# Kernel optimization log

Measured on AMD Instinct MI355X. Metric: run time of the kernel, lower is better.

The kernel has to match this reference:

```python
import jax, jax.numpy as jnp
import numpy as np

N_QUBITS = 8
DEPTH = 2
DIM = 2 ** N_QUBITS

# Hadamard gate (symmetric)
_H = (1.0 / np.sqrt(2.0)) * jnp.array([[1.0, 1.0], [1.0, -1.0]], dtype=jnp.complex64)
# sign table for <Z_i>: bit of wire i is bit (n-1-i) of the basis index (wire 0 = MSB)
_bits = (np.arange(DIM)[:, None] >> np.arange(N_QUBITS - 1, -1, -1)[None, :]) & 1
_SIGNS = jnp.asarray(1.0 - 2.0 * _bits, dtype=jnp.float32)  # [DIM, n_qubits]


def _quantum(ang):
    """Vectorized statevector simulation of the circuit:
    RX(ang_i) on each wire, then DEPTH x (CNOT ladder + H on last wire);
    returns <Z_i> for each wire. ang: [R, N_QUBITS] float32 -> [R, N_QUBITS]."""
    R = ang.shape[0]
    half = ang * 0.5
    a0 = jnp.cos(half).astype(jnp.complex64)
    a1 = (jnp.sin(half) * (-1j)).astype(jnp.complex64)  # RX|0> = cos|0> - i sin|1>
    single = jnp.stack([a0, a1], axis=-1)  # [R, n, 2]
    # product state via kron over qubits (wire 0 is the most significant factor)
    state = single[:, 0]  # [R, 2]
    for q in range(1, N_QUBITS):
        state = (state[:, :, None] * single[:, q][:, None, :]).reshape(R, -1)
    for _ in range(DEPTH):
        # CNOT ladder on adjacent wires (i -> i+1)
        for i in range(N_QUBITS - 1):
            s = state.reshape(R, 2 ** i, 2, 2, -1)  # [R, pre, ctrl, tgt, post]
            s = jnp.concatenate([s[:, :, :1], s[:, :, 1:, ::-1]], axis=2)
            state = s.reshape(R, -1)
        # Hadamard on the last wire
        s = state.reshape(R, -1, 2)
        state = (s @ _H).reshape(R, -1)
    probs = state.real ** 2 + state.imag ** 2  # [R, DIM]
    return probs @ _SIGNS  # [R, n_qubits]


def setup_inputs() -> dict:
    key = jax.random.key(0)
    k_x, k_w1, k_w2 = jax.random.split(key, 3)
    B, S, E, F = 8, 4096, 1024, N_QUBITS
    x = jax.random.normal(k_x, (B, S, E), dtype=jnp.float32)
    w1 = jax.random.normal(k_w1, (F, E), dtype=jnp.float32) * 0.02
    b1 = jnp.zeros((F,), dtype=jnp.float32)
    w2 = jax.random.normal(k_w2, (E, F), dtype=jnp.float32) * 0.02
    b2 = jnp.zeros((E,), dtype=jnp.float32)
    return {"x": x, "w1": w1, "b1": b1, "w2": w2, "b2": b2}


def reference(x, w1, b1, w2, b2):
    B, S, E = x.shape
    h = jnp.einsum('bse,fe->bsf', x, w1) + b1  # linear1 -> [B, S, ffn_dim]
    q = _quantum(h.reshape(-1, N_QUBITS)).reshape(B, S, N_QUBITS)
    # dropout is identity in eval mode
    return jnp.einsum('bsf,ef->bse', q, w2) + b2  # linear2 -> [B, S, E]
```

## Files before the change

kernel.cpp:

```cpp
#include <hip/hip_runtime.h>


constexpr int E       = 1024;
constexpr int R_TOTAL = 8 * 4096;
constexpr int ROWS_A  = 32;
constexpr int ROWS_B  = 16;

__global__ __launch_bounds__(256)
void ffq_qkernel(const float* __restrict__ x,
                 const float* __restrict__ w1,
                 const float* __restrict__ b1,
                 float* __restrict__ q)
{
    __shared__ float part[ROWS_A][33];

    const int t    = threadIdx.x;
    const int lane = t & 63;
    const int wid  = t >> 6;
    const int c0   = t * 4;

    float4 w1r[8];
#pragma unroll
    for (int f = 0; f < 8; ++f)
        w1r[f] = *(const float4*)(w1 + f * E + c0);

    const int row0 = blockIdx.x * ROWS_A;

    float4 xv = *(const float4*)(x + (size_t)row0 * E + c0);
    for (int s = 0; s < ROWS_A; ++s) {
        const float4 xc = xv;
        if (s + 1 < ROWS_A)
            xv = *(const float4*)(x + (size_t)(row0 + s + 1) * E + c0);

        float h[8];
#pragma unroll
        for (int f = 0; f < 8; ++f)
            h[f] = xc.x * w1r[f].x + xc.y * w1r[f].y
                 + xc.z * w1r[f].z + xc.w * w1r[f].w;

        {   const bool hb = lane & 1;
            float s0 = hb ? h[0] : h[4];
            float s1 = hb ? h[1] : h[5];
            float s2 = hb ? h[2] : h[6];
            float s3 = hb ? h[3] : h[7];
            s0 = __shfl_xor(s0, 1); s1 = __shfl_xor(s1, 1);
            s2 = __shfl_xor(s2, 1); s3 = __shfl_xor(s3, 1);
            h[0] = (hb ? h[4] : h[0]) + s0;
            h[1] = (hb ? h[5] : h[1]) + s1;
            h[2] = (hb ? h[6] : h[2]) + s2;
            h[3] = (hb ? h[7] : h[3]) + s3;
        }
        {   const bool hb = lane & 2;
            float s0 = hb ? h[0] : h[2];
            float s1 = hb ? h[1] : h[3];
            s0 = __shfl_xor(s0, 2); s1 = __shfl_xor(s1, 2);
            h[0] = (hb ? h[2] : h[0]) + s0;
            h[1] = (hb ? h[3] : h[1]) + s1;
        }
        float v;
        {   const bool hb = lane & 4;
            float s0 = hb ? h[0] : h[1];
            s0 = __shfl_xor(s0, 4);
            v = (hb ? h[1] : h[0]) + s0;
        }
        v += __shfl_xor(v, 8);
        v += __shfl_xor(v, 16);
        v += __shfl_xor(v, 32);

        if (lane < 8) {
            const int f = ((lane & 1) << 2) | (lane & 2) | ((lane >> 2) & 1);
            part[s][f * 4 + wid] = v;
        }
    }
    __syncthreads();

    {
        const int s = wid * 8 + (lane >> 3);
        const int f = lane & 7;
        const float hq = part[s][f * 4 + 0] + part[s][f * 4 + 1]
                       + part[s][f * 4 + 2] + part[s][f * 4 + 3] + b1[f];
        float p = __cosf(hq);
        float u = __shfl_up(p, 2, 8); if (f >= 2) p *= u;
        u = __shfl_up(p, 4, 8);       if (f >= 4) p *= u;
        const float p6 = __shfl(p, 6, 8);
        if (f == 7) p *= p6;
        q[(size_t)(row0 + s) * 8 + f] = p;
    }
}

__global__ __launch_bounds__(256)
void ffq_okernel(const float* __restrict__ q,
                 const float* __restrict__ w2,
                 const float* __restrict__ b2,
                 float* __restrict__ out)
{
    __shared__ __align__(16) float4 qsh[ROWS_B * 2];

    const int t  = threadIdx.x;
    const int c0 = t * 4;
    const int row0 = blockIdx.x * ROWS_B;

    if (t < ROWS_B * 2)
        qsh[t] = ((const float4*)(q + (size_t)row0 * 8))[t];

    float w2a[4][8];
#pragma unroll
    for (int j = 0; j < 4; ++j) {
        const float4 lo = *(const float4*)(w2 + (size_t)(c0 + j) * 8);
        const float4 hi = *(const float4*)(w2 + (size_t)(c0 + j) * 8 + 4);
        w2a[j][0] = lo.x; w2a[j][1] = lo.y; w2a[j][2] = lo.z; w2a[j][3] = lo.w;
        w2a[j][4] = hi.x; w2a[j][5] = hi.y; w2a[j][6] = hi.z; w2a[j][7] = hi.w;
    }
    const float4 b2v = *(const float4*)(b2 + c0);

    __syncthreads();

#pragma unroll 4
    for (int s = 0; s < ROWS_B; ++s) {
        const float4 qlo = qsh[2 * s];
        const float4 qhi = qsh[2 * s + 1];
        const float qv[8] = {qlo.x, qlo.y, qlo.z, qlo.w,
                             qhi.x, qhi.y, qhi.z, qhi.w};
        float4 o = b2v;
#pragma unroll
        for (int f = 0; f < 8; ++f) {
            o.x += qv[f] * w2a[0][f];
            o.y += qv[f] * w2a[1][f];
            o.z += qv[f] * w2a[2][f];
            o.w += qv[f] * w2a[3][f];
        }
        *(float4*)(out + (size_t)(row0 + s) * E + c0) = o;
    }
}

extern "C" void kernel_launch(void* const* d_in, const int* in_sizes, int n_in,
                              void* d_out, int out_size, void* d_ws, size_t ws_size,
                              hipStream_t stream)
{
    const float* x  = (const float*)d_in[0];
    const float* w1 = (const float*)d_in[1];
    const float* b1 = (const float*)d_in[2];
    const float* w2 = (const float*)d_in[3];
    const float* b2 = (const float*)d_in[4];
    float* out = (float*)d_out;
    float* q   = (float*)d_ws;

    ffq_qkernel<<<dim3(R_TOTAL / ROWS_A), 256, 0, stream>>>(x, w1, b1, q);
    ffq_okernel<<<dim3(R_TOTAL / ROWS_B), 256, 0, stream>>>(q, w2, b2, out);
}
```

Measured before the change: 270.6 us.

## Fuse projection, quantum stage and output projection into one kernel with batched prefetch

Merges the two kernels into one, so the per-row quantum features stay in shared memory and never pass through a global workspace. This removes one launch and the global write and read of q. It also prefetches x in batches of 8 rows instead of one row ahead, sets launch bounds to 4 blocks per SM, and caches b1 in shared memory. In exchange, each block now loads both w1 and w2 and keeps more registers live, which may limit occupancy.

```diff
diff --git a/kernel.cpp b/kernel.cpp
--- a/kernel.cpp
+++ b/kernel.cpp
@@ -1,107 +1,113 @@
 #include <hip/hip_runtime.h>
 
 
+constexpr int THREADS = 256;
+constexpr int TILE    = 32;
+constexpr int BATCH   = 8;
 constexpr int E       = 1024;
 constexpr int R_TOTAL = 8 * 4096;
-constexpr int ROWS_A  = 32;
-constexpr int ROWS_B  = 16;
 
-__global__ __launch_bounds__(256)
-void ffq_qkernel(const float* __restrict__ x,
-                 const float* __restrict__ w1,
-                 const float* __restrict__ b1,
-                 float* __restrict__ q)
+__global__ __launch_bounds__(THREADS, 4)
+void ffq_kernel(const float* __restrict__ x,
+                const float* __restrict__ w1,
+                const float* __restrict__ b1,
+                const float* __restrict__ w2,
+                const float* __restrict__ b2,
+                float* __restrict__ out)
 {
-    __shared__ float part[ROWS_A][33];
+    __shared__ float part[TILE][33];
+    __shared__ __align__(16) float qsh[TILE][8];
+    __shared__ float b1s[8];
 
     const int t    = threadIdx.x;
     const int lane = t & 63;
     const int wid  = t >> 6;
     const int c0   = t * 4;
 
+    if (t < 8) b1s[t] = b1[t];
+
     float4 w1r[8];
 #pragma unroll
     for (int f = 0; f < 8; ++f)
         w1r[f] = *(const float4*)(w1 + f * E + c0);
 
-    const int row0 = blockIdx.x * ROWS_A;
+    const int row0 = blockIdx.x * TILE;
 
-    float4 xv = *(const float4*)(x + (size_t)row0 * E + c0);
-    for (int s = 0; s < ROWS_A; ++s) {
-        const float4 xc = xv;
-        if (s + 1 < ROWS_A)
-            xv = *(const float4*)(x + (size_t)(row0 + s + 1) * E + c0);
+    float4 cur[BATCH];
+#pragma unroll
+    for (int s = 0; s < BATCH; ++s)
+        cur[s] = *(const float4*)(x + (size_t)(row0 + s) * E + c0);
 
-        float h[8];
 #pragma unroll
-        for (int f = 0; f < 8; ++f)
-            h[f] = xc.x * w1r[f].x + xc.y * w1r[f].y
-                 + xc.z * w1r[f].z + xc.w * w1r[f].w;
+    for (int b = 0; b < TILE / BATCH; ++b) {
+        float4 nxt[BATCH];
+        if (b + 1 < TILE / BATCH) {
+#pragma unroll
+            for (int s = 0; s < BATCH; ++s)
+                nxt[s] = *(const float4*)(x + (size_t)(row0 + (b + 1) * BATCH + s) * E + c0);
+        }
 
-        {   const bool hb = lane & 1;
-            float s0 = hb ? h[0] : h[4];
-            float s1 = hb ? h[1] : h[5];
-            float s2 = hb ? h[2] : h[6];
-            float s3 = hb ? h[3] : h[7];
-            s0 = __shfl_xor(s0, 1); s1 = __shfl_xor(s1, 1);
-            s2 = __shfl_xor(s2, 1); s3 = __shfl_xor(s3, 1);
-            h[0] = (hb ? h[4] : h[0]) + s0;
-            h[1] = (hb ? h[5] : h[1]) + s1;
-            h[2] = (hb ? h[6] : h[2]) + s2;
-            h[3] = (hb ? h[7] : h[3]) + s3;
+#pragma unroll
+        for (int s = 0; s < BATCH; ++s) {
+            const float4 xc = cur[s];
+            float h[8];
+#pragma unroll
+            for (int f = 0; f < 8; ++f)
+                h[f] = xc.x * w1r[f].x + xc.y * w1r[f].y
+                     + xc.z * w1r[f].z + xc.w * w1r[f].w;
+
+            {   const bool hb = lane & 1;
+                float s0 = hb ? h[0] : h[4];
+                float s1 = hb ? h[1] : h[5];
+                float s2 = hb ? h[2] : h[6];
+                float s3 = hb ? h[3] : h[7];
+                s0 = __shfl_xor(s0, 1); s1 = __shfl_xor(s1, 1);
+                s2 = __shfl_xor(s2, 1); s3 = __shfl_xor(s3, 1);
+                h[0] = (hb ? h[4] : h[0]) + s0;
+                h[1] = (hb ? h[5] : h[1]) + s1;
+                h[2] = (hb ? h[6] : h[2]) + s2;
+                h[3] = (hb ? h[7] : h[3]) + s3;
+            }
+            {   const bool hb = lane & 2;
+                float s0 = hb ? h[0] : h[2];
+                float s1 = hb ? h[1] : h[3];
+                s0 = __shfl_xor(s0, 2); s1 = __shfl_xor(s1, 2);
+                h[0] = (hb ? h[2] : h[0]) + s0;
+                h[1] = (hb ? h[3] : h[1]) + s1;
+            }
+            float v;
+            {   const bool hb = lane & 4;
+                float s0 = hb ? h[0] : h[1];
+                s0 = __shfl_xor(s0, 4);
+                v = (hb ? h[1] : h[0]) + s0;
+            }
+            v += __shfl_xor(v, 8);
+            v += __shfl_xor(v, 16);
+            v += __shfl_xor(v, 32);
+
+            if (lane < 8) {
+                const int f = ((lane & 1) << 2) | (lane & 2) | ((lane >> 2) & 1);
+                part[b * BATCH + s][f * 4 + wid] = v;
+            }
         }
-        {   const bool hb = lane & 2;
-            float s0 = hb ? h[0] : h[2];
-            float s1 = hb ? h[1] : h[3];
-            s0 = __shfl_xor(s0, 2); s1 = __shfl_xor(s1, 2);
-            h[0] = (hb ? h[2] : h[0]) + s0;
-            h[1] = (hb ? h[3] : h[1]) + s1;
-        }
-        float v;
-        {   const bool hb = lane & 4;
-            float s0 = hb ? h[0] : h[1];
-            s0 = __shfl_xor(s0, 4);
-            v = (hb ? h[1] : h[0]) + s0;
-        }
-        v += __shfl_xor(v, 8);
-        v += __shfl_xor(v, 16);
-        v += __shfl_xor(v, 32);
 
-        if (lane < 8) {
-            const int f = ((lane & 1) << 2) | (lane & 2) | ((lane >> 2) & 1);
-            part[s][f * 4 + wid] = v;
-        }
+#pragma unroll
+        for (int s = 0; s < BATCH; ++s) cur[s] = nxt[s];
     }
     __syncthreads();
 
     {
-        const int s = wid * 8 + (lane >> 3);
-        const int f = lane & 7;
-        const float hq = part[s][f * 4 + 0] + part[s][f * 4 + 1]
-                       + part[s][f * 4 + 2] + part[s][f * 4 + 3] + b1[f];
+        const int r = t >> 3;
+        const int f = t & 7;
+        const float hq = part[r][f * 4 + 0] + part[r][f * 4 + 1]
+                       + part[r][f * 4 + 2] + part[r][f * 4 + 3] + b1s[f];
         float p = __cosf(hq);
         float u = __shfl_up(p, 2, 8); if (f >= 2) p *= u;
         u = __shfl_up(p, 4, 8);       if (f >= 4) p *= u;
         const float p6 = __shfl(p, 6, 8);
         if (f == 7) p *= p6;
-        q[(size_t)(row0 + s) * 8 + f] = p;
+        qsh[r][f] = p;
     }
-}
-
-__global__ __launch_bounds__(256)
-void ffq_okernel(const float* __restrict__ q,
-                 const float* __restrict__ w2,
-                 const float* __restrict__ b2,
-                 float* __restrict__ out)
-{
-    __shared__ __align__(16) float4 qsh[ROWS_B * 2];
-
-    const int t  = threadIdx.x;
-    const int c0 = t * 4;
-    const int row0 = blockIdx.x * ROWS_B;
-
-    if (t < ROWS_B * 2)
-        qsh[t] = ((const float4*)(q + (size_t)row0 * 8))[t];
 
     float w2a[4][8];
 #pragma unroll
@@ -115,10 +121,10 @@
 
     __syncthreads();
 
-#pragma unroll 4
-    for (int s = 0; s < ROWS_B; ++s) {
-        const float4 qlo = qsh[2 * s];
-        const float4 qhi = qsh[2 * s + 1];
+#pragma unroll 8
+    for (int s = 0; s < TILE; ++s) {
+        const float4 qlo = *(const float4*)(&qsh[s][0]);
+        const float4 qhi = *(const float4*)(&qsh[s][4]);
         const float qv[8] = {qlo.x, qlo.y, qlo.z, qlo.w,
                              qhi.x, qhi.y, qhi.z, qhi.w};
         float4 o = b2v;
@@ -143,8 +149,6 @@
     const float* w2 = (const float*)d_in[3];
     const float* b2 = (const float*)d_in[4];
     float* out = (float*)d_out;
-    float* q   = (float*)d_ws;
 
-    ffq_qkernel<<<dim3(R_TOTAL / ROWS_A), 256, 0, stream>>>(x, w1, b1, q);
-    ffq_okernel<<<dim3(R_TOTAL / ROWS_B), 256, 0, stream>>>(q, w2, b2, out);
+    ffq_kernel<<<dim3(R_TOTAL / TILE), THREADS, 0, stream>>>(x, w1, b1, w2, b2, out);
 }
```

New measurement: 263.8 us. 1.03x faster.
